# Kernel optimization log

Hardware: AMD Instinct MI355X
Metric: run time of the kernel (lower is better)

The kernel has to match this reference:

```python
import jax, jax.numpy as jnp
import numpy as np

V = 50000   # words_num
D = 128     # embedding_dim
B = 2048    # batch
P = 20      # max Huffman path length


def setup_inputs() -> dict:
    key = jax.random.key(0)
    k1, k2, k3, k4, k5 = jax.random.split(key, 5)
    inputs_vector = jax.random.uniform(k1, (B, V), dtype=jnp.float32)
    path_nodes_indices = jax.random.randint(k2, (B, P), 0, V)
    huffman_codes = jax.random.randint(k3, (B, P), 0, 2).astype(jnp.float32)
    mask = jnp.ones((B, P), dtype=jnp.float32)
    # learned params, torch nn.Linear weight layout [out, in], kaiming-uniform-ish scale
    W_emb = jax.random.uniform(k4, (D, V), dtype=jnp.float32, minval=-1.0, maxval=1.0) / np.sqrt(V)
    W_cls = jax.random.uniform(k5, (V, D), dtype=jnp.float32, minval=-1.0, maxval=1.0) / np.sqrt(D)
    return {
        "inputs_vector": inputs_vector,
        "W_emb": W_emb,
        "W_cls": W_cls,
        "path_nodes_indices": path_nodes_indices,
        "huffman_codes": huffman_codes,
        "mask": mask,
    }


def _bce_with_logits(logits, targets):
    # numerically stable, elementwise (reduction='none')
    return jnp.maximum(logits, 0.0) - logits * targets + jnp.log1p(jnp.exp(-jnp.abs(logits)))


def reference(inputs_vector, W_emb, W_cls, path_nodes_indices, huffman_codes, mask):
    x = inputs_vector @ W_emb.T              # [B, D]  embedding Linear (no bias)
    logits_full = x @ W_cls.T                # [B, V]  full-vocab cls matmul (as in source)
    logits = jnp.take_along_axis(logits_full, path_nodes_indices, axis=1)  # [B, P]
    loss = _bce_with_logits(logits, huffman_codes)  # [B, P]
    masked_loss = loss * mask
    per_sample = masked_loss.sum(axis=-1) / mask.sum(axis=-1)  # [B]
    return per_sample.mean()
```

## Files before the change

### kernel.cpp

```cpp
#include <hip/hip_runtime.h>
#include <hip/hip_bf16.h>

#define V 50000
#define D 128
#define B 2048
#define P 20

#define BM 128
#define BN 128
#define BK 64
#define NSPLIT 56
#define KC 896
#define NMT (B / BM)

typedef float  f32x4   __attribute__((ext_vector_type(4)));
typedef short  bf16x8  __attribute__((ext_vector_type(8)));
typedef unsigned int uint4v __attribute__((ext_vector_type(4)));

__device__ __forceinline__ unsigned int pk2(float a, float b) {
    return (__float_as_uint(b) & 0xFFFF0000u) | (__float_as_uint(a) >> 16);
}

__global__ __launch_bounds__(256, 4)
void w2v_gemm_splitk(const float* __restrict__ Ain, const float* __restrict__ Wemb,
                     float* __restrict__ part, int use_atomic) {
    __shared__ unsigned short As[BM * BK];
    __shared__ unsigned short Ws[BN * BK];

    const int i     = blockIdx.x;
    const int xcd   = i & 7;
    const int j     = i >> 3;
    const int s     = xcd * 7 + (j >> 4);
    const int mtile = j & 15;
    const int m0    = mtile * BM;
    const int k0    = s * KC;
    const int k1    = (k0 + KC < V) ? (k0 + KC) : V;

    const int tid  = threadIdx.x;
    const int lane = tid & 63;
    const int wid  = tid >> 6;
    const int wr   = wid >> 1;
    const int wc   = wid & 1;

    f32x4 acc[4][4] = {};

    for (int ks = k0; ks < k1; ks += BK) {
#pragma unroll
        for (int t = 0; t < 8; ++t) {
            const int slot = tid + (t & 3) * 256;
            const int row  = slot >> 3;
            const int c8   = slot & 7;
            const int kg   = ks + c8 * 8;
            float4 v0 = make_float4(0.f, 0.f, 0.f, 0.f);
            float4 v1 = make_float4(0.f, 0.f, 0.f, 0.f);
            if (kg < k1) {
                const float* src = (t < 4) ? &Ain[(size_t)(m0 + row) * V + kg]
                                           : &Wemb[(size_t)row * V + kg];
                v0 = *reinterpret_cast<const float4*>(src);
                v1 = *reinterpret_cast<const float4*>(src + 4);
            }
            uint4v u;
            u.x = pk2(v0.x, v0.y);
            u.y = pk2(v0.z, v0.w);
            u.z = pk2(v1.x, v1.y);
            u.w = pk2(v1.z, v1.w);
            const unsigned dst = (unsigned)(row * 128) + (((unsigned)(c8 * 16)) ^ ((unsigned)(row & 7) << 4));
            char* base = (t < 4) ? (char*)As : (char*)Ws;
            *reinterpret_cast<uint4v*>(base + dst) = u;
        }
        __syncthreads();

#pragma unroll
        for (int kk = 0; kk < BK; kk += 32) {
            const unsigned kb = (unsigned)(kk * 2) + ((unsigned)(lane >> 4) << 4);
            bf16x8 af[4], wf[4];
#pragma unroll
            for (int m = 0; m < 4; ++m) {
                const int r = wr * 64 + m * 16 + (lane & 15);
                af[m] = *reinterpret_cast<const bf16x8*>((char*)As + r * 128 + (kb ^ ((unsigned)(r & 7) << 4)));
            }
#pragma unroll
            for (int n = 0; n < 4; ++n) {
                const int r = wc * 64 + n * 16 + (lane & 15);
                wf[n] = *reinterpret_cast<const bf16x8*>((char*)Ws + r * 128 + (kb ^ ((unsigned)(r & 7) << 4)));
            }
#pragma unroll
            for (int m = 0; m < 4; ++m)
#pragma unroll
                for (int n = 0; n < 4; ++n)
                    acc[m][n] = __builtin_amdgcn_mfma_f32_16x16x32_bf16(af[m], wf[n], acc[m][n], 0, 0, 0);
        }
        __syncthreads();
    }

    float* outp = use_atomic ? part : (part + (size_t)s * (B * D));
#pragma unroll
    for (int m = 0; m < 4; ++m) {
        int r0 = m0 + wr * 64 + m * 16 + (lane >> 4) * 4;
#pragma unroll
        for (int n = 0; n < 4; ++n) {
            int c0 = wc * 64 + n * 16 + (lane & 15);
#pragma unroll
            for (int jj = 0; jj < 4; ++jj) {
                float v = acc[m][n][jj];
                size_t off = (size_t)(r0 + jj) * D + c0;
                if (use_atomic) atomicAdd(&outp[off], v);
                else            outp[off] = v;
            }
        }
    }
}

__global__ __launch_bounds__(256)
void w2v_loss(const float* __restrict__ part, int nsplit,
              const float* __restrict__ Wcls, const int* __restrict__ pathIdx,
              const float* __restrict__ codes, const float* __restrict__ mask,
              float* __restrict__ out) {
    const int lane = threadIdx.x & 63;
    const int wid  = threadIdx.x >> 6;
    const int b    = blockIdx.x * 4 + wid;

    float x0 = 0.f, x1 = 0.f;
    for (int s = 0; s < nsplit; ++s) {
        const float2 v = *reinterpret_cast<const float2*>(&part[(size_t)s * (B * D) + (size_t)b * D + lane * 2]);
        x0 += v.x; x1 += v.y;
    }

    float lsum = 0.f, msum = 0.f;
#pragma unroll
    for (int p = 0; p < P; ++p) {
        int node = pathIdx[b * P + p];
        const float2 w = *reinterpret_cast<const float2*>(&Wcls[(size_t)node * D + lane * 2]);
        float d = x0 * w.x + x1 * w.y;
#pragma unroll
        for (int off = 1; off < 64; off <<= 1)
            d += __shfl_xor(d, off, 64);
        float t  = codes[b * P + p];
        float mm = mask[b * P + p];
        float loss = fmaxf(d, 0.f) - d * t + log1pf(__expf(-fabsf(d)));
        lsum += loss * mm;
        msum += mm;
    }
    float per = (msum > 0.f) ? (lsum / msum) : 0.f;

    __shared__ float wsum[4];
    if (lane == 0) wsum[wid] = per;
    __syncthreads();
    if (threadIdx.x == 0) {
        float ssum = wsum[0] + wsum[1] + wsum[2] + wsum[3];
        atomicAdd(out, ssum * (1.0f / (float)B));
    }
}

extern "C" void kernel_launch(void* const* d_in, const int* in_sizes, int n_in,
                              void* d_out, int out_size, void* d_ws, size_t ws_size,
                              hipStream_t stream) {
    const float* inputs = (const float*)d_in[0];
    const float* W_emb  = (const float*)d_in[1];
    const float* W_cls  = (const float*)d_in[2];
    const int*   path   = (const int*)  d_in[3];
    const float* codes  = (const float*)d_in[4];
    const float* mask   = (const float*)d_in[5];
    float* out = (float*)d_out;

    const size_t part_need = (size_t)NSPLIT * B * D * sizeof(float);
    const int use_atomic = (ws_size < part_need) ? 1 : 0;
    float* part = (float*)d_ws;
    const int nsplit_eff = use_atomic ? 1 : NSPLIT;

    if (use_atomic)
        hipMemsetAsync(d_ws, 0, (size_t)B * D * sizeof(float), stream);
    hipMemsetAsync(d_out, 0, sizeof(float), stream);

    w2v_gemm_splitk<<<dim3(NMT * NSPLIT), dim3(256), 0, stream>>>(inputs, W_emb, part, use_atomic);
    w2v_loss<<<dim3(B / 4), dim3(256), 0, stream>>>(part, nsplit_eff, W_cls, path, codes, mask, out);
}
```

Baseline: 162.4 us.

## Store split-K partials as bf16 via LDS-staged coalesced writes with nontemporal loads

The split-K GEMM now rounds its per-split partial sums to bf16, stages them through shared memory, and writes them out with coalesced 16-byte nontemporal stores. This halves the size of the partial buffer that is written and then re-read by the loss kernel. The streamed input matrix is also read with nontemporal loads so it does not crowd the cache. The trade-off is extra rounding error from storing 56 partials in bf16 before summation, plus an extra LDS round-trip and barrier in the epilogue.

Measured after the change: 175.2 us. +7.9%, slower.

```diff
diff --git a/kernel.cpp b/kernel.cpp
--- a/kernel.cpp
+++ b/kernel.cpp
@@ -20,12 +20,17 @@
 __device__ __forceinline__ unsigned int pk2(float a, float b) {
     return (__float_as_uint(b) & 0xFFFF0000u) | (__float_as_uint(a) >> 16);
 }
+__device__ __forceinline__ unsigned short f2bf(float f) {
+    unsigned int u = __float_as_uint(f);
+    return (unsigned short)((u + 0x7FFFu + ((u >> 16) & 1u)) >> 16);
+}
 
 __global__ __launch_bounds__(256, 4)
 void w2v_gemm_splitk(const float* __restrict__ Ain, const float* __restrict__ Wemb,
-                     float* __restrict__ part, int use_atomic) {
-    __shared__ unsigned short As[BM * BK];
-    __shared__ unsigned short Ws[BN * BK];
+                     void* __restrict__ part, int use_atomic) {
+    __shared__ unsigned short Sm[2 * BM * BK];
+    unsigned short* As = Sm;
+    unsigned short* Ws = Sm + BM * BK;
 
     const int i     = blockIdx.x;
     const int xcd   = i & 7;
@@ -51,19 +56,24 @@
             const int row  = slot >> 3;
             const int c8   = slot & 7;
             const int kg   = ks + c8 * 8;
-            float4 v0 = make_float4(0.f, 0.f, 0.f, 0.f);
-            float4 v1 = make_float4(0.f, 0.f, 0.f, 0.f);
+            f32x4 v0 = {0.f, 0.f, 0.f, 0.f};
+            f32x4 v1 = {0.f, 0.f, 0.f, 0.f};
             if (kg < k1) {
-                const float* src = (t < 4) ? &Ain[(size_t)(m0 + row) * V + kg]
-                                           : &Wemb[(size_t)row * V + kg];
-                v0 = *reinterpret_cast<const float4*>(src);
-                v1 = *reinterpret_cast<const float4*>(src + 4);
+                if (t < 4) {
+                    const f32x4* src = reinterpret_cast<const f32x4*>(&Ain[(size_t)(m0 + row) * V + kg]);
+                    v0 = __builtin_nontemporal_load(src);
+                    v1 = __builtin_nontemporal_load(src + 1);
+                } else {
+                    const f32x4* src = reinterpret_cast<const f32x4*>(&Wemb[(size_t)row * V + kg]);
+                    v0 = src[0];
+                    v1 = src[1];
+                }
             }
             uint4v u;
-            u.x = pk2(v0.x, v0.y);
-            u.y = pk2(v0.z, v0.w);
-            u.z = pk2(v1.x, v1.y);
-            u.w = pk2(v1.z, v1.w);
+            u.x = pk2(v0[0], v0[1]);
+            u.y = pk2(v0[2], v0[3]);
+            u.z = pk2(v1[0], v1[1]);
+            u.w = pk2(v1[2], v1[3]);
             const unsigned dst = (unsigned)(row * 128) + (((unsigned)(c8 * 16)) ^ ((unsigned)(row & 7) << 4));
             char* base = (t < 4) ? (char*)As : (char*)Ws;
             *reinterpret_cast<uint4v*>(base + dst) = u;
@@ -93,26 +103,44 @@
         __syncthreads();
     }
 
-    float* outp = use_atomic ? part : (part + (size_t)s * (B * D));
+    if (use_atomic) {
+        float* outp = (float*)part;
+#pragma unroll
+        for (int m = 0; m < 4; ++m) {
+            int r0 = m0 + wr * 64 + m * 16 + (lane >> 4) * 4;
+#pragma unroll
+            for (int n = 0; n < 4; ++n) {
+                int c0 = wc * 64 + n * 16 + (lane & 15);
+#pragma unroll
+                for (int jj = 0; jj < 4; ++jj)
+                    atomicAdd(&outp[(size_t)(r0 + jj) * D + c0], acc[m][n][jj]);
+            }
+        }
+        return;
+    }
 #pragma unroll
     for (int m = 0; m < 4; ++m) {
-        int r0 = m0 + wr * 64 + m * 16 + (lane >> 4) * 4;
+        int r0 = wr * 64 + m * 16 + (lane >> 4) * 4;
 #pragma unroll
         for (int n = 0; n < 4; ++n) {
             int c0 = wc * 64 + n * 16 + (lane & 15);
 #pragma unroll
-            for (int jj = 0; jj < 4; ++jj) {
-                float v = acc[m][n][jj];
-                size_t off = (size_t)(r0 + jj) * D + c0;
-                if (use_atomic) atomicAdd(&outp[off], v);
-                else            outp[off] = v;
-            }
-        }
+            for (int jj = 0; jj < 4; ++jj)
+                Sm[(r0 + jj) * 128 + c0] = f2bf(acc[m][n][jj]);
+        }
+    }
+    __syncthreads();
+    char* dstb = (char*)part + ((size_t)s * B + m0) * (D * 2);
+#pragma unroll
+    for (int it = 0; it < 8; ++it) {
+        const int off = (it * 256 + tid) * 16;
+        uint4v v = *reinterpret_cast<const uint4v*>((char*)Sm + off);
+        __builtin_nontemporal_store(v, reinterpret_cast<uint4v*>(dstb + off));
     }
 }
 
 __global__ __launch_bounds__(256)
-void w2v_loss(const float* __restrict__ part, int nsplit,
+void w2v_loss(const void* __restrict__ part, int nsplit, int part_bf16,
               const float* __restrict__ Wcls, const int* __restrict__ pathIdx,
               const float* __restrict__ codes, const float* __restrict__ mask,
               float* __restrict__ out) {
@@ -121,9 +149,17 @@
     const int b    = blockIdx.x * 4 + wid;
 
     float x0 = 0.f, x1 = 0.f;
-    for (int s = 0; s < nsplit; ++s) {
-        const float2 v = *reinterpret_cast<const float2*>(&part[(size_t)s * (B * D) + (size_t)b * D + lane * 2]);
-        x0 += v.x; x1 += v.y;
+    if (part_bf16) {
+        const unsigned* pb = (const unsigned*)part;
+        for (int s = 0; s < nsplit; ++s) {
+            unsigned u = __builtin_nontemporal_load(&pb[((size_t)s * B + b) * 64 + lane]);
+            x0 += __uint_as_float(u << 16);
+            x1 += __uint_as_float(u & 0xFFFF0000u);
+        }
+    } else {
+        const float* pf = (const float*)part;
+        const float2 v = *reinterpret_cast<const float2*>(&pf[(size_t)b * D + lane * 2]);
+        x0 = v.x; x1 = v.y;
     }
 
     float lsum = 0.f, msum = 0.f;
@@ -163,15 +199,15 @@
     const float* mask   = (const float*)d_in[5];
     float* out = (float*)d_out;
 
-    const size_t part_need = (size_t)NSPLIT * B * D * sizeof(float);
+    const size_t part_need = (size_t)NSPLIT * B * D * sizeof(unsigned short);
     const int use_atomic = (ws_size < part_need) ? 1 : 0;
-    float* part = (float*)d_ws;
     const int nsplit_eff = use_atomic ? 1 : NSPLIT;
 
     if (use_atomic)
         hipMemsetAsync(d_ws, 0, (size_t)B * D * sizeof(float), stream);
     hipMemsetAsync(d_out, 0, sizeof(float), stream);
 
-    w2v_gemm_splitk<<<dim3(NMT * NSPLIT), dim3(256), 0, stream>>>(inputs, W_emb, part, use_atomic);
-    w2v_loss<<<dim3(B / 4), dim3(256), 0, stream>>>(part, nsplit_eff, W_cls, path, codes, mask, out);
-}
+    w2v_gemm_splitk<<<dim3(NMT * NSPLIT), dim3(256), 0, stream>>>(inputs, W_emb, d_ws, use_atomic);
+    w2v_loss<<<dim3(B / 4), dim3(256), 0, stream>>>(d_ws, nsplit_eff, use_atomic ? 0 : 1,
+                                                    W_cls, path, codes, mask, out);
+}
```
